# Kernel tuning notes

Measured on AMD Instinct MI355X. Metric: run time of the kernel, lower is better.

## Reference

```python
import jax, jax.numpy as jnp
import numpy as np

OUT_H = 7
OUT_W = 7
RATIO = 2  # sampling_ratio (static)


def _roi_align(feat, boxes, out_h, out_w, sx, sy, ratio):
    """torchvision-style RoIAlign (aligned=False) on a single image.
    feat: [C,H,W], boxes: [N,4] (x1,y1,x2,y2) in image coords.
    sx, sy: spatial scales (W_feat/W_img, H_feat/H_img). Returns [N,C,out_h,out_w]."""
    C, H, W = feat.shape
    N = boxes.shape[0]
    x1 = boxes[:, 0] * sx
    y1 = boxes[:, 1] * sy
    x2 = boxes[:, 2] * sx
    y2 = boxes[:, 3] * sy
    rw = jnp.maximum(x2 - x1, 1.0)
    rh = jnp.maximum(y2 - y1, 1.0)
    bw = rw / out_w
    bh = rh / out_h
    offs = (jnp.arange(ratio, dtype=feat.dtype) + 0.5) / ratio  # sub-bin sample offsets
    # sample coordinates: [N, out*ratio]
    gy = y1[:, None, None] + (jnp.arange(out_h, dtype=feat.dtype)[None, :, None] + offs[None, None, :]) * bh[:, None, None]
    gx = x1[:, None, None] + (jnp.arange(out_w, dtype=feat.dtype)[None, :, None] + offs[None, None, :]) * bw[:, None, None]
    Y = gy.reshape(N, out_h * ratio)
    X = gx.reshape(N, out_w * ratio)
    vy = (Y >= -1.0) & (Y <= H)
    vx = (X >= -1.0) & (X <= W)
    Yc = jnp.clip(Y, 0.0, H - 1)
    Xc = jnp.clip(X, 0.0, W - 1)
    y0 = jnp.floor(Yc).astype(jnp.int32)
    x0 = jnp.floor(Xc).astype(jnp.int32)
    y1i = jnp.minimum(y0 + 1, H - 1)
    x1i = jnp.minimum(x0 + 1, W - 1)
    ly = Yc - y0.astype(Yc.dtype)
    lx = Xc - x0.astype(Xc.dtype)
    hy = 1.0 - ly
    hx = 1.0 - lx

    def g(yi, xi):  # corner gather -> [C, N, out_h*ratio, out_w*ratio]
        return feat[:, yi[:, :, None], xi[:, None, :]]

    val = (hy[:, :, None] * hx[:, None, :]) * g(y0, x0) \
        + (hy[:, :, None] * lx[:, None, :]) * g(y0, x1i) \
        + (ly[:, :, None] * hx[:, None, :]) * g(y1i, x0) \
        + (ly[:, :, None] * lx[:, None, :]) * g(y1i, x1i)
    valid = vy[:, :, None] & vx[:, None, :]
    val = jnp.where(valid[None], val, 0.0)
    # average over the ratio x ratio sampling grid (always divide by ratio^2)
    val = val.reshape(C, N, out_h, ratio, out_w, ratio).mean(axis=(3, 5))
    return val.transpose(1, 0, 2, 3)


def setup_inputs() -> dict:
    key = jax.random.key(0)
    k0, k1, k2, kb = jax.random.split(key, 4)
    img_h, img_w = 800, 1216
    feat0 = jax.random.normal(k0, (1, 256, 200, 304), dtype=jnp.float32)
    feat1 = jax.random.normal(k1, (1, 256, 100, 152), dtype=jnp.float32)
    feat2 = jax.random.normal(k2, (1, 256, 50, 76), dtype=jnp.float32)
    u = jax.random.uniform(kb, (256, 4), dtype=jnp.float32)
    bx1 = u[:, 0] * (img_w - 32)
    by1 = u[:, 1] * (img_h - 32)
    bw = 16.0 + u[:, 2] * 256.0
    bh = 16.0 + u[:, 3] * 256.0
    bx2 = jnp.minimum(bx1 + bw, float(img_w))
    by2 = jnp.minimum(by1 + bh, float(img_h))
    boxes = jnp.stack([bx1, by1, bx2, by2], axis=1)
    return {"feat0": feat0, "feat1": feat1, "feat2": feat2, "boxes": boxes,
            "img_h": img_h, "img_w": img_w}


def reference(feat0, feat1, feat2, boxes, img_h, img_w):
    _, C, H, W = feat0.shape
    # upsample coarser levels by 2**i, half-pixel bilinear == torch align_corners=False
    ups = [feat0]
    for i, f in enumerate([feat1, feat2], 1):
        s = 2 ** i
        ups.append(jax.image.resize(
            f, (f.shape[0], f.shape[1], f.shape[2] * s, f.shape[3] * s), method='bilinear'))
    fused = jnp.concatenate(ups, axis=1)[0]  # [3C, H, W] (single image)
    sx = W / img_w
    sy = H / img_h
    return _roi_align(fused, boxes, OUT_H, OUT_W, sx, sy, RATIO)
```

## Files before the change

kernel.cpp:

```cpp
#include <hip/hip_runtime.h>
#include <hip/hip_bf16.h>

#define H0 200
#define W0 304
#define H1 100
#define W1 152
#define H2 50
#define W2 76
#define CPL 256
#define CTOT 768
#define OH 7
#define OW 7
#define NPOS 49
#define SROW 264

#define P0 (H0*W0)
#define P1 (H1*W1)
#define P2 (H2*W2)
#define T0_OFF ((size_t)0)
#define T1_OFF ((size_t)P0*CPL)
#define T2_OFF ((size_t)P0*CPL + (size_t)P1*CPL)
#define WS_ELEMS ((size_t)P0*CPL + (size_t)P1*CPL + (size_t)P2*CPL)
#define WS_BYTES (WS_ELEMS * 2)

__device__ __forceinline__ float hat01(float d) {
    return fmaxf(0.0f, 1.0f - fabsf(d));
}

__device__ __forceinline__ unsigned short f2bf_rne(float x) {
    unsigned int u = __float_as_uint(x);
    u += 0x7fffu + ((u >> 16) & 1u);
    return (unsigned short)(u >> 16);
}

__global__ void __launch_bounds__(256)
transpose_all_kernel(const float* __restrict__ f0, const float* __restrict__ f1,
                     const float* __restrict__ f2,
                     unsigned short* __restrict__ T0,
                     unsigned short* __restrict__ T1,
                     unsigned short* __restrict__ T2, int n0, int n01) {
    __shared__ unsigned short tile[64][72];
    int b = blockIdx.x;
    const float* in; unsigned short* outp; int P; int rel;
    if (b < n0)       { in = f0; outp = T0; P = P0; rel = b; }
    else if (b < n01) { in = f1; outp = T1; P = P1; rel = b - n0; }
    else              { in = f2; outp = T2; P = P2; rel = b - n01; }
    int p0 = (rel >> 2) * 64;
    int c0 = (rel & 3) * 64;

    int q = threadIdx.x & 15;
    int r = threadIdx.x >> 4;
    bool full = (p0 + 64 <= P);
#pragma unroll
    for (int i = 0; i < 4; ++i) {
        int c = c0 + r + 16 * i;
        int p = p0 + 4 * q;
        float4 v;
        if (full) {
            v = *(const float4*)(in + (size_t)c * P + p);
        } else {
            v.x = (p + 0 < P) ? in[(size_t)c * P + p + 0] : 0.0f;
            v.y = (p + 1 < P) ? in[(size_t)c * P + p + 1] : 0.0f;
            v.z = (p + 2 < P) ? in[(size_t)c * P + p + 2] : 0.0f;
            v.w = (p + 3 < P) ? in[(size_t)c * P + p + 3] : 0.0f;
        }
        tile[4 * q + 0][r + 16 * i] = f2bf_rne(v.x);
        tile[4 * q + 1][r + 16 * i] = f2bf_rne(v.y);
        tile[4 * q + 2][r + 16 * i] = f2bf_rne(v.z);
        tile[4 * q + 3][r + 16 * i] = f2bf_rne(v.w);
    }
    __syncthreads();
    int q8 = threadIdx.x & 7;
    int r8 = threadIdx.x >> 3;
#pragma unroll
    for (int i = 0; i < 2; ++i) {
        int p = p0 + r8 + 32 * i;
        if (p < P) {
            uint4 w = *(const uint4*)&tile[r8 + 32 * i][8 * q8];
            *(uint4*)(outp + (size_t)p * CPL + c0 + 8 * q8) = w;
        }
    }
}

template<int TY, int TX>
__device__ __forceinline__ void run_level_pair(const unsigned short* __restrict__ Tc,
                                               const int (*s_idx)[6], const float (*s_w)[6],
                                               float (*sout)[SROW], int wv, int half, int l) {
    for (int pp = wv; pp < 25; pp += 8) {
        int pos = 2 * pp + half;
        pos = (pos > NPOS - 1) ? (NPOS - 1) : pos;
        int oh = pos / 7;
        int ow = pos - oh * 7;
        int yi[TY], xi[TX];
        float yw[TY], xw[TX];
#pragma unroll
        for (int j = 0; j < TY; ++j) { yi[j] = s_idx[oh][j];     yw[j] = s_w[oh][j]; }
#pragma unroll
        for (int j = 0; j < TX; ++j) { xi[j] = s_idx[7 + ow][j]; xw[j] = s_w[7 + ow][j]; }

        float a0 = 0.f, a1 = 0.f, a2 = 0.f, a3 = 0.f;
        float a4 = 0.f, a5 = 0.f, a6 = 0.f, a7 = 0.f;
#pragma unroll
        for (int a = 0; a < TY; ++a) {
            float s0 = 0.f, s1 = 0.f, s2 = 0.f, s3 = 0.f;
            float s4 = 0.f, s5 = 0.f, s6 = 0.f, s7 = 0.f;
#pragma unroll
            for (int b = 0; b < TX; ++b) {
                uint4 v = *(const uint4*)(Tc + (unsigned)(yi[a] + xi[b]));
                float wxb = xw[b];
                s0 += wxb * __uint_as_float(v.x << 16);
                s1 += wxb * __uint_as_float(v.x & 0xffff0000u);
                s2 += wxb * __uint_as_float(v.y << 16);
                s3 += wxb * __uint_as_float(v.y & 0xffff0000u);
                s4 += wxb * __uint_as_float(v.z << 16);
                s5 += wxb * __uint_as_float(v.z & 0xffff0000u);
                s6 += wxb * __uint_as_float(v.w << 16);
                s7 += wxb * __uint_as_float(v.w & 0xffff0000u);
            }
            float wya = yw[a];
            a0 += wya * s0; a1 += wya * s1; a2 += wya * s2; a3 += wya * s3;
            a4 += wya * s4; a5 += wya * s5; a6 += wya * s6; a7 += wya * s7;
        }
        float4 r0, r1;
        r0.x = a0 * 0.25f; r0.y = a1 * 0.25f; r0.z = a2 * 0.25f; r0.w = a3 * 0.25f;
        r1.x = a4 * 0.25f; r1.y = a5 * 0.25f; r1.z = a6 * 0.25f; r1.w = a7 * 0.25f;
        *(float4*)&sout[pos][8 * l + 0] = r0;
        *(float4*)&sout[pos][8 * l + 4] = r1;
    }
}

__global__ void __launch_bounds__(512)
roi_align_cl7_kernel(const unsigned short* __restrict__ T0,
                     const unsigned short* __restrict__ T1,
                     const unsigned short* __restrict__ T2,
                     const float* __restrict__ boxes,
                     const int* __restrict__ img_h_p,
                     const int* __restrict__ img_w_p,
                     float* __restrict__ out) {
    __shared__ float sout[NPOS][SROW];
    __shared__ int   s_idx[14][6];
    __shared__ float s_w[14][6];

    int n = blockIdx.x;
    int level = blockIdx.y;
    const unsigned short* T; int Hc, Wc; float inv_s;
    if (level == 0)      { T = T0; Hc = H0; Wc = W0; inv_s = 1.0f;  }
    else if (level == 1) { T = T1; Hc = H1; Wc = W1; inv_s = 0.5f;  }
    else                 { T = T2; Hc = H2; Wc = W2; inv_s = 0.25f; }

    int tid = threadIdx.x;
    if (tid < 14) {
        int axis = (tid >= 7) ? 1 : 0;
        int o = tid - axis * 7;
        float sx = (float)W0 / (float)img_w_p[0];
        float sy = (float)H0 / (float)img_h_p[0];
        float a1, bs; int Hf, Hca, mul;
        if (axis) {
            a1 = boxes[n * 4 + 0] * sx;
            float a2 = boxes[n * 4 + 2] * sx;
            bs = fmaxf(a2 - a1, 1.0f) * (1.0f / (float)OW);
            Hf = W0; Hca = Wc; mul = 1;
        } else {
            a1 = boxes[n * 4 + 1] * sy;
            float a2 = boxes[n * 4 + 3] * sy;
            bs = fmaxf(a2 - a1, 1.0f) * (1.0f / (float)OH);
            Hf = H0; Hca = Hc; mul = Wc;
        }
        int idx[6]; float w[6];
#pragma unroll
        for (int j = 0; j < 6; ++j) { idx[j] = 0; w[j] = 0.0f; }
        if (level == 0) {
#pragma unroll
            for (int r2 = 0; r2 < 2; ++r2) {
                float Y = a1 + ((float)o + 0.25f + 0.5f * (float)r2) * bs;
                float v = (Y >= -1.0f && Y <= (float)Hf) ? 1.0f : 0.0f;
                float Yc = fminf(fmaxf(Y, 0.0f), (float)(Hf - 1));
                int y0 = (int)Yc; float lf = Yc - (float)y0;
                idx[2 * r2]     = y0;                  w[2 * r2]     = (1.0f - lf) * v;
                idx[2 * r2 + 1] = min(y0 + 1, Hf - 1); w[2 * r2 + 1] = lf * v;
            }
        } else {
            int bases[2]; float w3[2][3];
#pragma unroll
            for (int r2 = 0; r2 < 2; ++r2) {
                float Y = a1 + ((float)o + 0.25f + 0.5f * (float)r2) * bs;
                float v = (Y >= -1.0f && Y <= (float)Hf) ? 1.0f : 0.0f;
                float Yc = fminf(fmaxf(Y, 0.0f), (float)(Hf - 1));
                int y0 = (int)Yc; float lf = Yc - (float)y0; float hf = 1.0f - lf;
                int yf1 = min(y0 + 1, Hf - 1);
                float yc0 = fminf(fmaxf(((float)y0 + 0.5f) * inv_s - 0.5f, 0.0f), (float)(Hca - 1));
                float yc1 = fminf(fmaxf(((float)yf1 + 0.5f) * inv_s - 0.5f, 0.0f), (float)(Hca - 1));
                int b2 = (int)yc0;
                bases[r2] = b2;
#pragma unroll
                for (int t2 = 0; t2 < 3; ++t2) {
                    float j2 = (float)(b2 + t2);
                    w3[r2][t2] = v * (hf * hat01(yc0 - j2) + lf * hat01(yc1 - j2));
                }
            }
            int dmax = (level == 1) ? 3 : 2;
            int d = min(max(bases[1] - bases[0], 0), dmax);
            w[0] += w3[0][0]; w[1] += w3[0][1]; w[2] += w3[0][2];
            w[d] += w3[1][0]; w[d + 1] += w3[1][1]; w[d + 2] += w3[1][2];
#pragma unroll
            for (int j = 0; j < 6; ++j) idx[j] = min(bases[0] + j, Hca - 1);
        }
#pragma unroll
        for (int j = 0; j < 6; ++j) { s_idx[tid][j] = idx[j] * mul * CPL; s_w[tid][j] = w[j]; }
    }
    __syncthreads();

    int lane = tid & 63;
    int wv = tid >> 6;
    int half = (lane >> 5) & 1;
    int l = lane & 31;
    const unsigned short* Tc = T + l * 8;

    if (level == 0)      run_level_pair<4, 4>(Tc, s_idx, s_w, sout, wv, half, l);
    else if (level == 1) run_level_pair<6, 6>(Tc, s_idx, s_w, sout, wv, half, l);
    else                 run_level_pair<5, 5>(Tc, s_idx, s_w, sout, wv, half, l);
    __syncthreads();

    size_t obase = ((size_t)n * CTOT + (size_t)level * CPL) * NPOS;
    for (int i2 = tid; i2 < CPL * NPOS; i2 += 512) {
        int c = i2 / NPOS;
        int p = i2 - c * NPOS;
        out[obase + i2] = sout[p][c];
    }
}

__device__ __forceinline__ void axis_w3_fb(int yf0, int Hf, int Hc, float inv_s,
                                           float lf, int& base, float* w) {
    int yf1 = min(yf0 + 1, Hf - 1);
    float hf = 1.0f - lf;
    float yc0 = fminf(fmaxf(((float)yf0 + 0.5f) * inv_s - 0.5f, 0.0f), (float)(Hc - 1));
    float yc1 = fminf(fmaxf(((float)yf1 + 0.5f) * inv_s - 0.5f, 0.0f), (float)(Hc - 1));
    base = (int)yc0;
#pragma unroll
    for (int r = 0; r < 3; ++r) {
        float j = (float)(base + r);
        w[r] = hf * hat01(yc0 - j) + lf * hat01(yc1 - j);
    }
}

__global__ void __launch_bounds__(256)
roi_align_fused_fb_kernel(const float* __restrict__ f0,
                          const float* __restrict__ f1,
                          const float* __restrict__ f2,
                          const float* __restrict__ boxes,
                          const int* __restrict__ img_h_p,
                          const int* __restrict__ img_w_p,
                          float* __restrict__ out,
                          int total) {
    int i = blockIdx.x * blockDim.x + threadIdx.x;
    if (i >= total) return;
    int ow = i % OW;
    int t = i / OW;
    int oh = t % OH; t /= OH;
    int c = t % CTOT;
    int n = t / CTOT;
    float sx = (float)W0 / (float)img_w_p[0];
    float sy = (float)H0 / (float)img_h_p[0];
    float bx1 = boxes[n * 4 + 0] * sx;
    float by1 = boxes[n * 4 + 1] * sy;
    float bw = fmaxf(boxes[n * 4 + 2] * sx - bx1, 1.0f) / OW;
    float bh = fmaxf(boxes[n * 4 + 3] * sy - by1, 1.0f) / OH;
    int level = c >> 8;
    int cl = c & (CPL - 1);
    const float* f;
    int Hc, Wc; float inv_s;
    if (level == 0)      { f = f0 + (size_t)cl * P0; Hc = H0; Wc = W0; inv_s = 1.0f;  }
    else if (level == 1) { f = f1 + (size_t)cl * P1; Hc = H1; Wc = W1; inv_s = 0.5f;  }
    else                 { f = f2 + (size_t)cl * P2; Hc = H2; Wc = W2; inv_s = 0.25f; }
    float acc = 0.0f;
#pragma unroll
    for (int ry = 0; ry < 2; ++ry) {
        float Y = by1 + ((float)oh + 0.25f + 0.5f * ry) * bh;
        bool vy = (Y >= -1.0f) && (Y <= (float)H0);
        float Yc = fminf(fmaxf(Y, 0.0f), (float)(H0 - 1));
        int y0 = (int)Yc;
        float ly = Yc - (float)y0;
#pragma unroll
        for (int rx = 0; rx < 2; ++rx) {
            float X = bx1 + ((float)ow + 0.25f + 0.5f * rx) * bw;
            bool vx = (X >= -1.0f) && (X <= (float)W0);
            float Xc = fminf(fmaxf(X, 0.0f), (float)(W0 - 1));
            int x0 = (int)Xc;
            float lx = Xc - (float)x0;
            float v;
            if (level == 0) {
                int y1i = min(y0 + 1, H0 - 1), x1i = min(x0 + 1, W0 - 1);
                float hy = 1.0f - ly, hx = 1.0f - lx;
                float v00 = f[y0 * W0 + x0],  v01 = f[y0 * W0 + x1i];
                float v10 = f[y1i * W0 + x0], v11 = f[y1i * W0 + x1i];
                v = hy * (hx * v00 + lx * v01) + ly * (hx * v10 + lx * v11);
            } else {
                int yb, xb; float wy[3], wxl[3];
                axis_w3_fb(y0, H0, Hc, inv_s, ly, yb, wy);
                axis_w3_fb(x0, W0, Wc, inv_s, lx, xb, wxl);
                v = 0.0f;
#pragma unroll
                for (int a = 0; a < 3; ++a) {
                    int row = min(yb + a, Hc - 1) * Wc;
                    float s = 0.0f;
#pragma unroll
                    for (int b = 0; b < 3; ++b)
                        s += wxl[b] * f[row + min(xb + b, Wc - 1)];
                    v += wy[a] * s;
                }
            }
            if (vy && vx) acc += v;
        }
    }
    out[i] = acc * 0.25f;
}

extern "C" void kernel_launch(void* const* d_in, const int* in_sizes, int n_in,
                              void* d_out, int out_size, void* d_ws, size_t ws_size,
                              hipStream_t stream) {
    const float* f0    = (const float*)d_in[0];
    const float* f1    = (const float*)d_in[1];
    const float* f2    = (const float*)d_in[2];
    const float* boxes = (const float*)d_in[3];
    const int* img_h_p = (const int*)d_in[4];
    const int* img_w_p = (const int*)d_in[5];
    float* out = (float*)d_out;
    int N = in_sizes[3] / 4;

    if (ws_size >= WS_BYTES) {
        unsigned short* ws = (unsigned short*)d_ws;
        unsigned short* T0 = ws + T0_OFF;
        unsigned short* T1 = ws + T1_OFF;
        unsigned short* T2 = ws + T2_OFF;
        int n0 = ((P0 + 63) / 64) * 4;
        int n1 = ((P1 + 63) / 64) * 4;
        int n2 = ((P2 + 63) / 64) * 4;
        transpose_all_kernel<<<n0 + n1 + n2, 256, 0, stream>>>(
            f0, f1, f2, T0, T1, T2, n0, n0 + n1);
        roi_align_cl7_kernel<<<dim3(N, 3), 512, 0, stream>>>(
            T0, T1, T2, boxes, img_h_p, img_w_p, out);
    } else {
        int total = N * CTOT * OH * OW;
        roi_align_fused_fb_kernel<<<(total + 255) / 256, 256, 0, stream>>>(
            f0, f1, f2, boxes, img_h_p, img_w_p, out, total);
    }
}
```

Measured before the change: 160.2 us.

## Switch staging to fp16 with packed half2 FMAs and per-row ROI blocks

The transposed channel-last staging buffer now holds fp16 instead of bf16. The inner x-direction interpolation uses packed __hfma2 on half2 pairs rather than unpacking to fp32. The ROI kernel is regridded from one block per (box, level) to one block per (box, output row), covering all three levels with 256 threads and a smaller shared buffer, which should raise occupancy. The changes aim to cut ALU unpack work and improve parallelism. In exchange, fp16 accumulation in the inner sum reduces precision and fp16 has a narrower range than bf16.

```diff
diff --git a/kernel.cpp b/kernel.cpp
--- a/kernel.cpp
+++ b/kernel.cpp
@@ -1,5 +1,5 @@
 #include <hip/hip_runtime.h>
-#include <hip/hip_bf16.h>
+#include <hip/hip_fp16.h>
 
 #define H0 200
 #define W0 304
@@ -12,7 +12,7 @@
 #define OH 7
 #define OW 7
 #define NPOS 49
-#define SROW 264
+#define SROW2 772
 
 #define P0 (H0*W0)
 #define P1 (H1*W1)
@@ -27,10 +27,8 @@
     return fmaxf(0.0f, 1.0f - fabsf(d));
 }
 
-__device__ __forceinline__ unsigned short f2bf_rne(float x) {
-    unsigned int u = __float_as_uint(x);
-    u += 0x7fffu + ((u >> 16) & 1u);
-    return (unsigned short)(u >> 16);
+__device__ __forceinline__ unsigned short f2h_rne(float x) {
+    return __half_as_ushort(__float2half_rn(x));
 }
 
 __global__ void __launch_bounds__(256)
@@ -64,10 +62,10 @@
             v.z = (p + 2 < P) ? in[(size_t)c * P + p + 2] : 0.0f;
             v.w = (p + 3 < P) ? in[(size_t)c * P + p + 3] : 0.0f;
         }
-        tile[4 * q + 0][r + 16 * i] = f2bf_rne(v.x);
-        tile[4 * q + 1][r + 16 * i] = f2bf_rne(v.y);
-        tile[4 * q + 2][r + 16 * i] = f2bf_rne(v.z);
-        tile[4 * q + 3][r + 16 * i] = f2bf_rne(v.w);
+        tile[4 * q + 0][r + 16 * i] = f2h_rne(v.x);
+        tile[4 * q + 1][r + 16 * i] = f2h_rne(v.y);
+        tile[4 * q + 2][r + 16 * i] = f2h_rne(v.z);
+        tile[4 * q + 3][r + 16 * i] = f2h_rne(v.w);
     }
     __syncthreads();
     int q8 = threadIdx.x & 7;
@@ -83,96 +81,93 @@
 }
 
 template<int TY, int TX>
-__device__ __forceinline__ void run_level_pair(const unsigned short* __restrict__ Tc,
-                                               const int (*s_idx)[6], const float (*s_w)[6],
-                                               float (*sout)[SROW], int wv, int half, int l) {
-    for (int pp = wv; pp < 25; pp += 8) {
-        int pos = 2 * pp + half;
-        pos = (pos > NPOS - 1) ? (NPOS - 1) : pos;
-        int oh = pos / 7;
-        int ow = pos - oh * 7;
-        int yi[TY], xi[TX];
-        float yw[TY], xw[TX];
-#pragma unroll
-        for (int j = 0; j < TY; ++j) { yi[j] = s_idx[oh][j];     yw[j] = s_w[oh][j]; }
-#pragma unroll
-        for (int j = 0; j < TX; ++j) { xi[j] = s_idx[7 + ow][j]; xw[j] = s_w[7 + ow][j]; }
-
-        float a0 = 0.f, a1 = 0.f, a2 = 0.f, a3 = 0.f;
-        float a4 = 0.f, a5 = 0.f, a6 = 0.f, a7 = 0.f;
-#pragma unroll
-        for (int a = 0; a < TY; ++a) {
-            float s0 = 0.f, s1 = 0.f, s2 = 0.f, s3 = 0.f;
-            float s4 = 0.f, s5 = 0.f, s6 = 0.f, s7 = 0.f;
-#pragma unroll
-            for (int b = 0; b < TX; ++b) {
-                uint4 v = *(const uint4*)(Tc + (unsigned)(yi[a] + xi[b]));
-                float wxb = xw[b];
-                s0 += wxb * __uint_as_float(v.x << 16);
-                s1 += wxb * __uint_as_float(v.x & 0xffff0000u);
-                s2 += wxb * __uint_as_float(v.y << 16);
-                s3 += wxb * __uint_as_float(v.y & 0xffff0000u);
-                s4 += wxb * __uint_as_float(v.z << 16);
-                s5 += wxb * __uint_as_float(v.z & 0xffff0000u);
-                s6 += wxb * __uint_as_float(v.w << 16);
-                s7 += wxb * __uint_as_float(v.w & 0xffff0000u);
-            }
-            float wya = yw[a];
-            a0 += wya * s0; a1 += wya * s1; a2 += wya * s2; a3 += wya * s3;
-            a4 += wya * s4; a5 += wya * s5; a6 += wya * s6; a7 += wya * s7;
-        }
-        float4 r0, r1;
-        r0.x = a0 * 0.25f; r0.y = a1 * 0.25f; r0.z = a2 * 0.25f; r0.w = a3 * 0.25f;
-        r1.x = a4 * 0.25f; r1.y = a5 * 0.25f; r1.z = a6 * 0.25f; r1.w = a7 * 0.25f;
-        *(float4*)&sout[pos][8 * l + 0] = r0;
-        *(float4*)&sout[pos][8 * l + 4] = r1;
-    }
-}
-
-__global__ void __launch_bounds__(512)
-roi_align_cl7_kernel(const unsigned short* __restrict__ T0,
-                     const unsigned short* __restrict__ T1,
-                     const unsigned short* __restrict__ T2,
+__device__ __forceinline__ void proc_level(const __half* __restrict__ T,
+                                           const int (*__restrict__ sidx)[6],
+                                           const float (*__restrict__ sw)[6],
+                                           float* __restrict__ srow,
+                                           unsigned co, int ow) {
+    unsigned yo[TY]; float yw[TY];
+#pragma unroll
+    for (int j = 0; j < TY; ++j) { yo[j] = (unsigned)sidx[0][j]; yw[j] = sw[0][j]; }
+    unsigned xo[TX]; __half2 xw2[TX];
+#pragma unroll
+    for (int j = 0; j < TX; ++j) {
+        xo[j] = (unsigned)sidx[1 + ow][j];
+        xw2[j] = __float2half2_rn(sw[1 + ow][j]);
+    }
+    float a0 = 0.f, a1 = 0.f, a2 = 0.f, a3 = 0.f;
+    float a4 = 0.f, a5 = 0.f, a6 = 0.f, a7 = 0.f;
+#pragma unroll
+    for (int a = 0; a < TY; ++a) {
+        unsigned ro = yo[a] + co;
+        __half2 r0 = __float2half2_rn(0.0f);
+        __half2 r1 = r0, r2 = r0, r3 = r0;
+#pragma unroll
+        for (int b = 0; b < TX; ++b) {
+            uint4 v = *(const uint4*)(T + (ro + xo[b]));
+            r0 = __hfma2(xw2[b], *(const __half2*)&v.x, r0);
+            r1 = __hfma2(xw2[b], *(const __half2*)&v.y, r1);
+            r2 = __hfma2(xw2[b], *(const __half2*)&v.z, r2);
+            r3 = __hfma2(xw2[b], *(const __half2*)&v.w, r3);
+        }
+        float wa = yw[a];
+        a0 = fmaf(wa, __low2float(r0), a0);  a1 = fmaf(wa, __high2float(r0), a1);
+        a2 = fmaf(wa, __low2float(r1), a2);  a3 = fmaf(wa, __high2float(r1), a3);
+        a4 = fmaf(wa, __low2float(r2), a4);  a5 = fmaf(wa, __high2float(r2), a5);
+        a6 = fmaf(wa, __low2float(r3), a6);  a7 = fmaf(wa, __high2float(r3), a7);
+    }
+    float4 o0, o1;
+    o0.x = a0 * 0.25f; o0.y = a1 * 0.25f; o0.z = a2 * 0.25f; o0.w = a3 * 0.25f;
+    o1.x = a4 * 0.25f; o1.y = a5 * 0.25f; o1.z = a6 * 0.25f; o1.w = a7 * 0.25f;
+    *(float4*)(srow + co) = o0;
+    *(float4*)(srow + co + 4) = o1;
+}
+
+__global__ void __launch_bounds__(256, 6)
+roi_align_row_kernel(const unsigned short* __restrict__ T0p,
+                     const unsigned short* __restrict__ T1p,
+                     const unsigned short* __restrict__ T2p,
                      const float* __restrict__ boxes,
                      const int* __restrict__ img_h_p,
                      const int* __restrict__ img_w_p,
                      float* __restrict__ out) {
-    __shared__ float sout[NPOS][SROW];
-    __shared__ int   s_idx[14][6];
-    __shared__ float s_w[14][6];
-
-    int n = blockIdx.x;
-    int level = blockIdx.y;
-    const unsigned short* T; int Hc, Wc; float inv_s;
-    if (level == 0)      { T = T0; Hc = H0; Wc = W0; inv_s = 1.0f;  }
-    else if (level == 1) { T = T1; Hc = H1; Wc = W1; inv_s = 0.5f;  }
-    else                 { T = T2; Hc = H2; Wc = W2; inv_s = 0.25f; }
-
-    int tid = threadIdx.x;
-    if (tid < 14) {
-        int axis = (tid >= 7) ? 1 : 0;
-        int o = tid - axis * 7;
+    __shared__ float sout[OW][SROW2];
+    __shared__ int   s_idx[3][8][6];
+    __shared__ float s_w[3][8][6];
+
+    const int n = blockIdx.x;
+    const int oh = blockIdx.y;
+    const int tid = threadIdx.x;
+
+    if (tid < 24) {
+        int lev = tid >> 3;
+        int o8 = tid & 7;
+        int axis = (o8 > 0) ? 1 : 0;
+        int o = axis ? (o8 - 1) : oh;
+        int Hc = (lev == 0) ? H0 : (lev == 1) ? H1 : H2;
+        int Wc = (lev == 0) ? W0 : (lev == 1) ? W1 : W2;
+        float inv_s = (lev == 0) ? 1.0f : (lev == 1) ? 0.5f : 0.25f;
         float sx = (float)W0 / (float)img_w_p[0];
         float sy = (float)H0 / (float)img_h_p[0];
-        float a1, bs; int Hf, Hca, mul;
+        float a1v, bs; int Hf, Hca, mul;
         if (axis) {
-            a1 = boxes[n * 4 + 0] * sx;
-            float a2 = boxes[n * 4 + 2] * sx;
-            bs = fmaxf(a2 - a1, 1.0f) * (1.0f / (float)OW);
+            a1v = boxes[n * 4 + 0] * sx;
+            float a2v = boxes[n * 4 + 2] * sx;
+            bs = fmaxf(a2v - a1v, 1.0f) * (1.0f / (float)OW);
             Hf = W0; Hca = Wc; mul = 1;
         } else {
-            a1 = boxes[n * 4 + 1] * sy;
-            float a2 = boxes[n * 4 + 3] * sy;
-            bs = fmaxf(a2 - a1, 1.0f) * (1.0f / (float)OH);
+            a1v = boxes[n * 4 + 1] * sy;
+            float a2v = boxes[n * 4 + 3] * sy;
+            bs = fmaxf(a2v - a1v, 1.0f) * (1.0f / (float)OH);
             Hf = H0; Hca = Hc; mul = Wc;
         }
         int idx[6]; float w[6];
 #pragma unroll
         for (int j = 0; j < 6; ++j) { idx[j] = 0; w[j] = 0.0f; }
-        if (level == 0) {
+        if (lev == 0) {
 #pragma unroll
             for (int r2 = 0; r2 < 2; ++r2) {
-                float Y = a1 + ((float)o + 0.25f + 0.5f * (float)r2) * bs;
+                float Y = a1v + ((float)o + 0.25f + 0.5f * (float)r2) * bs;
                 float v = (Y >= -1.0f && Y <= (float)Hf) ? 1.0f : 0.0f;
                 float Yc = fminf(fmaxf(Y, 0.0f), (float)(Hf - 1));
                 int y0 = (int)Yc; float lf = Yc - (float)y0;
@@ -183,7 +178,7 @@
             int bases[2]; float w3[2][3];
 #pragma unroll
             for (int r2 = 0; r2 < 2; ++r2) {
-                float Y = a1 + ((float)o + 0.25f + 0.5f * (float)r2) * bs;
+                float Y = a1v + ((float)o + 0.25f + 0.5f * (float)r2) * bs;
                 float v = (Y >= -1.0f && Y <= (float)Hf) ? 1.0f : 0.0f;
                 float Yc = fminf(fmaxf(Y, 0.0f), (float)(Hf - 1));
                 int y0 = (int)Yc; float lf = Yc - (float)y0; float hf = 1.0f - lf;
@@ -198,7 +193,7 @@
                     w3[r2][t2] = v * (hf * hat01(yc0 - j2) + lf * hat01(yc1 - j2));
                 }
             }
-            int dmax = (level == 1) ? 3 : 2;
+            int dmax = (lev == 1) ? 3 : 2;
             int d = min(max(bases[1] - bases[0], 0), dmax);
             w[0] += w3[0][0]; w[1] += w3[0][1]; w[2] += w3[0][2];
             w[d] += w3[1][0]; w[d + 1] += w3[1][1]; w[d + 2] += w3[1][2];
@@ -206,26 +201,29 @@
             for (int j = 0; j < 6; ++j) idx[j] = min(bases[0] + j, Hca - 1);
         }
 #pragma unroll
-        for (int j = 0; j < 6; ++j) { s_idx[tid][j] = idx[j] * mul * CPL; s_w[tid][j] = w[j]; }
+        for (int j = 0; j < 6; ++j) { s_idx[lev][o8][j] = idx[j] * mul * CPL; s_w[lev][o8][j] = w[j]; }
     }
     __syncthreads();
 
-    int lane = tid & 63;
-    int wv = tid >> 6;
-    int half = (lane >> 5) & 1;
-    int l = lane & 31;
-    const unsigned short* Tc = T + l * 8;
-
-    if (level == 0)      run_level_pair<4, 4>(Tc, s_idx, s_w, sout, wv, half, l);
-    else if (level == 1) run_level_pair<6, 6>(Tc, s_idx, s_w, sout, wv, half, l);
-    else                 run_level_pair<5, 5>(Tc, s_idx, s_w, sout, wv, half, l);
+    const int lane = tid & 63;
+    const int wv = tid >> 6;
+    const int half = lane >> 5;
+    const int l = lane & 31;
+    int ow = 2 * wv + half;
+    ow = (ow > OW - 1) ? (OW - 1) : ow;
+    unsigned co = (unsigned)(l * 8);
+    float* srow = &sout[ow][0];
+
+    proc_level<4, 4>((const __half*)T0p, s_idx[0], s_w[0], srow,           co, ow);
+    proc_level<6, 6>((const __half*)T1p, s_idx[1], s_w[1], srow + CPL,     co, ow);
+    proc_level<5, 5>((const __half*)T2p, s_idx[2], s_w[2], srow + 2 * CPL, co, ow);
     __syncthreads();
 
-    size_t obase = ((size_t)n * CTOT + (size_t)level * CPL) * NPOS;
-    for (int i2 = tid; i2 < CPL * NPOS; i2 += 512) {
-        int c = i2 / NPOS;
-        int p = i2 - c * NPOS;
-        out[obase + i2] = sout[p][c];
+    size_t obase = (size_t)n * CTOT * NPOS + (size_t)oh * OW;
+    for (int i2 = tid; i2 < CTOT * OW; i2 += 256) {
+        int c = i2 / OW;
+        int p = i2 - c * OW;
+        out[obase + (size_t)c * NPOS + p] = sout[p][c];
     }
 }
 
@@ -337,7 +335,7 @@
         int n2 = ((P2 + 63) / 64) * 4;
         transpose_all_kernel<<<n0 + n1 + n2, 256, 0, stream>>>(
             f0, f1, f2, T0, T1, T2, n0, n0 + n1);
-        roi_align_cl7_kernel<<<dim3(N, 3), 512, 0, stream>>>(
+        roi_align_row_kernel<<<dim3(N, OH), 256, 0, stream>>>(
             T0, T1, T2, boxes, img_h_p, img_w_p, out);
     } else {
         int total = N * CTOT * OH * OW;
```

New measurement: 177.7 us. 10.9% more time.
